# Performance work log

Measured on AMD Instinct MI355X. Metric: run time of the kernel, lower is better.

## Reference

```python
import jax, jax.numpy as jnp
import numpy as np

SR = 22050
HOP = 512
BINS_PER_OCTAVE = 24
N_OCTAVES = 7
N_BINS = BINS_PER_OCTAVE * N_OCTAVES  # 168
FMIN = 32.7  # center_bins with bins_per_semitone=1 leaves fmin unchanged


def _make_cqt_kernels():
    """Right-aligned (causal) complex CQT kernels, 24 bins/octave, 7 octaves.

    This is the explicit math the stateful SlidingCqt24 C++ routine computes
    incrementally: for each bin k with center freq f_k = fmin * 2^(k/24),
    a Hann-windowed complex exponential of length N_k = ceil(Q*sr/f_k),
    Q = 1/(2^(1/24)-1). Bins are ordered ascending in frequency, matching the
    per-octave np.flip layout of the original forward.
    """
    Q = 1.0 / (2.0 ** (1.0 / BINS_PER_OCTAVE) - 1.0)
    freqs = FMIN * 2.0 ** (np.arange(N_BINS) / BINS_PER_OCTAVE)
    lens = np.ceil(Q * SR / freqs).astype(np.int64)
    n_max = int(lens.max())  # 23014
    kr = np.zeros((N_BINS, n_max), dtype=np.float32)
    ki = np.zeros((N_BINS, n_max), dtype=np.float32)
    for k in range(N_BINS):  # small fixed loop over 168 bins (setup only)
        n = int(lens[k])
        t = np.arange(n)
        win = np.hanning(n)
        c = win * np.exp(2j * np.pi * freqs[k] * t / SR) / n
        kr[k, n_max - n:] = c.real.astype(np.float32)
        ki[k, n_max - n:] = c.imag.astype(np.float32)
    return kr, ki


def setup_inputs() -> dict:
    key = jax.random.key(0)
    audio = jax.random.normal(key, (4, 1, 352768), dtype=jnp.float32)
    kr, ki = _make_cqt_kernels()
    return {
        "audio_waveforms": audio,
        "kern_real": jnp.asarray(kr),
        "kern_imag": jnp.asarray(ki),
    }


def reference(audio_waveforms, kern_real, kern_imag):
    # audio: [B, C, S]; kernels: [K, Nmax]
    n_max = kern_real.shape[1]
    B, C, S = audio_waveforms.shape
    n_blocks = S // HOP  # 689
    # Causal sliding window: block i analyzes the n_max samples ending at
    # sample (i+1)*HOP (left zero-pad for early blocks), matching the
    # block-streaming behavior of the sliding CQT.
    pad = n_max - HOP
    x = jnp.pad(audio_waveforms, ((0, 0), (0, 0), (pad, 0)))
    # Strided frame gather: [n_blocks, Nmax] index table.
    idx = jnp.arange(n_blocks)[:, None] * HOP + jnp.arange(n_max)[None, :]
    frames = x[..., idx]  # [B, C, T, Nmax]
    re = jnp.einsum("bctn,kn->bctk", frames, kern_real)
    im = jnp.einsum("bctn,kn->bctk", frames, kern_imag)
    mag = jnp.sqrt(re * re + im * im)  # [B, C, n_blocks, n_bins]
    return mag
```

## Files before the change

### kernel.cpp

```cpp
#include <hip/hip_runtime.h>
#include <math.h>


namespace {
constexpr int kSR    = 22050;
constexpr int kHop   = 512;
constexpr int kBins  = 168;
constexpr int kT     = 689;
constexpr int kB     = 4;
constexpr int kS     = 352768;
constexpr float kKScale    = 4096.0f;
constexpr float kKScaleInv = 1.0f / 4096.0f;
constexpr int kG16 = 11;
constexpr int kAcc = kB * kT * kBins * 2;
constexpr int kTPadB   = 768;
constexpr int kBinPadB = 176;
constexpr int kAccB    = kB * kTPadB * kBinPadB * 2;
}

typedef _Float16 half8 __attribute__((ext_vector_type(8)));
typedef _Float16 half2v __attribute__((ext_vector_type(2)));
typedef float floatx4 __attribute__((ext_vector_type(4)));

struct Jobs {
  int k0[48];
  int lo[48];
  int hi[48];
  int n;
};

struct JobsC {
  int lo16[kG16];
  int cb16[kG16];
  int mlo[3];
  int sm[12];
  int slo[12];
  int shi[12];
  int ns;
  int totch;
};

__device__ inline void atomAddF(float* p, float v) {
  __hip_atomic_fetch_add(p, v, __ATOMIC_RELAXED, __HIP_MEMORY_SCOPE_AGENT);
}

typedef __attribute__((address_space(3))) unsigned int lds_uint;
typedef __attribute__((address_space(1))) const unsigned int glb_uint;
__device__ __forceinline__ void dma16(const void* g, void* l) {
  __builtin_amdgcn_global_load_lds((glb_uint*)g, (lds_uint*)l, 16, 0, 0);
}

__global__ __launch_bounds__(256) void prep_fused(
    const float* __restrict__ x, const float* __restrict__ kr,
    const float* __restrict__ ki, _Float16* __restrict__ xp,
    _Float16* __restrict__ bp, float* __restrict__ accb,
    const int pad, const int xps, const int nmax,
    const int nbx, const int nbp, const JobsC jt) {
  int bid = blockIdx.x;
  const int tid = threadIdx.x;

  if (bid < nbx) {
    const int halfx = xps >> 1;
    const int gid = bid * 256 + tid;
    if (gid >= kB * halfx) return;
    const int b = gid / halfx;
    const int i = (gid - b * halfx) * 2;
    float v0 = 0.f, v1 = 0.f;
    if (i     >= pad && i     < pad + kS) v0 = x[(size_t)b * kS + (i - pad)];
    if (i + 1 >= pad && i + 1 < pad + kS) v1 = x[(size_t)b * kS + (i + 1 - pad)];
    half2v h; h.x = (_Float16)v0; h.y = (_Float16)v1;
    *(half2v*)&xp[(size_t)b * xps + i] = h;
    return;
  }
  bid -= nbx;

  if (bid < nbp) {
    const int chunkid = bid * 4 + (tid >> 6);
    const int lane = tid & 63;
    if (chunkid >= jt.totch) return;
    int g = 0;
    #pragma unroll
    for (int j = 1; j < kG16; ++j)
      if (chunkid >= jt.cb16[j]) g = j;
    const int c = chunkid - jt.cb16[g];
    const int mm = lane & 15;
    const int q  = lane >> 4;
    const int bin  = g * 16 + mm;
    const int col0 = jt.lo16[g] + c * 32 + q * 8;
    const bool binok = (bin < kBins);
    const float* rowr = kr + (size_t)bin * nmax;
    const float* rowi = ki + (size_t)bin * nmax;
    half8 hre, him;
    #pragma unroll
    for (int j = 0; j < 8; ++j) {
      const int col = col0 + j;
      const bool ok = binok && (col < nmax);
      hre[j] = ok ? (_Float16)(rowr[col] * kKScale) : (_Float16)0.f;
      him[j] = ok ? (_Float16)(rowi[col] * kKScale) : (_Float16)0.f;
    }
    _Float16* dst = bp + (size_t)chunkid * 1024 + lane * 8;
    *(half8*)dst = hre;
    *(half8*)(dst + 512) = him;
    return;
  }
  bid -= nbp;

  const int idx = (bid * 256 + tid) * 4;
  if (idx < kAcc)
    *(floatx4*)&accb[idx] = (floatx4){0.f, 0.f, 0.f, 0.f};
}

__global__ __launch_bounds__(256) void cqt_mfma7(
    const _Float16* __restrict__ bp, const _Float16* __restrict__ xp,
    float* __restrict__ accb, const int xps, const JobsC jt) {
  __shared__ _Float16 lds[2][12288];

  const int sx = blockIdx.y;
  const int fb = blockIdx.x >> 2;
  const int b  = blockIdx.x & 3;
  const int tid  = threadIdx.x;
  const int wave = tid >> 6;
  const int lane = tid & 63;
  const int mm = lane & 15;
  const int q  = lane >> 4;
  const int mac = jt.sm[sx];
  const int g16 = mac * 4 + wave;
  const bool gvalid = (g16 < kG16);
  const int mlo = jt.mlo[mac];
  const int gs = gvalid ? ((jt.lo16[g16] - mlo) >> 5) : 0x7fffffff;
  const int slo = jt.slo[sx];
  const int shi = jt.shi[sx];
  const int fbase = fb * 64;

  const _Float16* xb = xp + (size_t)b * xps;
  const int i0 = wave * 2;
  int aoff[2];
  #pragma unroll
  for (int j = 0; j < 2; ++j) {
    const int idx = i0 + j;
    const int tl = idx & 3;
    int row = fbase + tl * 16 + mm;
    if (row > kT - 1) row = kT - 1;
    aoff[j] = row * kHop + q * 8 + ((idx >> 2) * 32);
  }
  const _Float16* bgrp =
      gvalid ? (bp + (size_t)(jt.cb16[g16] - gs) * 1024 + lane * 8) : bp;

  floatx4 accr[4], acci[4];
  #pragma unroll
  for (int tl = 0; tl < 4; ++tl) {
    accr[tl] = (floatx4){0.f, 0.f, 0.f, 0.f};
    acci[tl] = (floatx4){0.f, 0.f, 0.f, 0.f};
  }

  auto stageDMA = [&](int c, int buf) {
    _Float16* L = lds[buf];
    #pragma unroll
    for (int j = 0; j < 2; ++j)
      dma16(xb + mlo + c * 32 + aoff[j], L + (i0 + j) * 512);
    if (gvalid && c >= gs) {
      const _Float16* bs = bgrp + (size_t)c * 1024;
      #pragma unroll
      for (int cc = 0; cc < 2; ++cc)
        #pragma unroll
        for (int ri = 0; ri < 2; ++ri)
          dma16(bs + cc * 1024 + ri * 512,
                L + 4096 + (wave * 4 + cc * 2 + ri) * 512);
    }
  };

  auto compute = [&](int c, int buf) {
    if (!gvalid || c < gs) return;
    const _Float16* L = lds[buf];
    #pragma unroll
    for (int cc = 0; cc < 2; ++cc) {
      const half8 Bre = *(const half8*)(L + 4096 + (wave * 4 + cc * 2) * 512 + lane * 8);
      const half8 Bim = *(const half8*)(L + 4096 + (wave * 4 + cc * 2 + 1) * 512 + lane * 8);
      #pragma unroll
      for (int tl = 0; tl < 4; ++tl) {
        const half8 A = *(const half8*)(L + (cc * 4 + tl) * 512 + lane * 8);
        accr[tl] = __builtin_amdgcn_mfma_f32_16x16x32_f16(A, Bre, accr[tl], 0, 0, 0);
        acci[tl] = __builtin_amdgcn_mfma_f32_16x16x32_f16(A, Bim, acci[tl], 0, 0, 0);
      }
    }
  };

  stageDMA(slo, 0);
  int buf = 0;
  #pragma unroll 1
  for (int c = slo; c < shi; c += 2) {
    __syncthreads();
    if (c + 2 < shi) stageDMA(c + 2, buf ^ 1);
    compute(c, buf);
    buf ^= 1;
  }

  const int bin = g16 * 16 + mm;
  if (bin < kBins) {
    #pragma unroll
    for (int tl = 0; tl < 4; ++tl) {
      const int tb = fbase + tl * 16 + q * 4;
      #pragma unroll
      for (int r = 0; r < 4; ++r) {
        const int t = tb + r;
        if (t < kT) {
          const size_t o = (((size_t)b * kT + t) * kBins + bin) * 2;
          atomAddF(&accb[o],     accr[tl][r] * kKScaleInv);
          atomAddF(&accb[o + 1], acci[tl][r] * kKScaleInv);
        }
      }
    }
  }
}

__global__ __launch_bounds__(256) void cqt_mag_final(
    const float* __restrict__ accb, float* __restrict__ out,
    const int tp, const int kp) {
  int gid = blockIdx.x * 256 + threadIdx.x;
  if (gid >= kB * kT * kBins) return;
  const int k = gid % kBins;
  const int r = gid / kBins;
  const int t = r % kT;
  const int b = r / kT;
  const float2 v = ((const float2*)accb)[((size_t)b * tp + t) * kp + k];
  out[gid] = sqrtf(v.x * v.x + v.y * v.y);
}

__global__ __launch_bounds__(256) void prep_x_kernel(
    const float* __restrict__ x, _Float16* __restrict__ xp,
    const int pad, const int xps) {
  const int halfx = xps >> 1;
  int gid = blockIdx.x * 256 + threadIdx.x;
  if (gid >= kB * halfx) return;
  const int b = gid / halfx;
  const int i = (gid - b * halfx) * 2;
  float v0 = 0.f, v1 = 0.f;
  if (i     >= pad && i     < pad + kS) v0 = x[(size_t)b * kS + (i - pad)];
  if (i + 1 >= pad && i + 1 < pad + kS) v1 = x[(size_t)b * kS + (i + 1 - pad)];
  half2v h; h.x = (_Float16)v0; h.y = (_Float16)v1;
  *(half2v*)&xp[(size_t)b * xps + i] = h;
}

__global__ __launch_bounds__(256) void cqt_mfma_kernel(
    const float* __restrict__ kr, const float* __restrict__ ki,
    const _Float16* __restrict__ xp, float* __restrict__ accb,
    const int nmax, const int xps, const Jobs jt) {
  __shared__ _Float16 Bs[2][16][264];
  const int jb = blockIdx.x;
  const int k0   = jt.k0[jb];
  const int n_lo = jt.lo[jb];
  const int n_hi = jt.hi[jb];
  const int b  = blockIdx.z;
  const int fb = blockIdx.y;
  const int tid  = threadIdx.x;
  const int lane = tid & 63;
  const int wave = tid >> 6;
  const int m = lane & 15;
  const int q = lane >> 4;
  const int sbin = tid >> 4;
  const int scol = tid & 15;
  const int gbin = k0 + sbin;
  const bool binok = (gbin < kBins);
  const float* rowr = kr + (size_t)gbin * nmax;
  const float* rowi = ki + (size_t)gbin * nmax;
  const int fbase = fb * 256 + wave * 64;
  const _Float16* ax =
      xp + (size_t)b * xps + (size_t)(fbase + m) * kHop + q * 8;
  floatx4 accr[4], acci[4];
  #pragma unroll
  for (int tl = 0; tl < 4; ++tl) {
    accr[tl] = (floatx4){0.f, 0.f, 0.f, 0.f};
    acci[tl] = (floatx4){0.f, 0.f, 0.f, 0.f};
  }
  for (int n0r = n_lo; n0r < n_hi; n0r += 256) {
    __syncthreads();
    #pragma unroll
    for (int c = 0; c < 16; ++c) {
      const int col = n0r + scol + c * 16;
      const bool ok = binok && (col < nmax);
      const float vr = ok ? rowr[col] : 0.f;
      const float vi = ok ? rowi[col] : 0.f;
      Bs[0][sbin][scol + c * 16] = (_Float16)(vr * kKScale);
      Bs[1][sbin][scol + c * 16] = (_Float16)(vi * kKScale);
    }
    __syncthreads();
    const _Float16* axr = ax + n0r;
    #pragma unroll
    for (int c = 0; c < 8; ++c) {
      const int ko = c * 32 + q * 8;
      const half8 br = *(const half8*)&Bs[0][m][ko];
      const half8 bi = *(const half8*)&Bs[1][m][ko];
      #pragma unroll
      for (int tl = 0; tl < 4; ++tl) {
        const half8 a = *(const half8*)(axr + tl * 16 * kHop + c * 32);
        accr[tl] = __builtin_amdgcn_mfma_f32_16x16x32_f16(a, br, accr[tl], 0, 0, 0);
        acci[tl] = __builtin_amdgcn_mfma_f32_16x16x32_f16(a, bi, acci[tl], 0, 0, 0);
      }
    }
  }
  #pragma unroll
  for (int tl = 0; tl < 4; ++tl) {
    #pragma unroll
    for (int rr = 0; rr < 4; ++rr) {
      const int t = fbase + tl * 16 + q * 4 + rr;
      const size_t o = (((size_t)b * kTPadB + t) * kBinPadB + (k0 + m)) * 2;
      atomAddF(&accb[o],     accr[tl][rr] * kKScaleInv);
      atomAddF(&accb[o + 1], acci[tl][rr] * kKScaleInv);
    }
  }
}

namespace fb32 {
constexpr int TT = 8;
constexpr int KG = 4;
constexpr int kTTiles  = (kT + TT - 1) / TT;
constexpr int kKGroups = kBins / KG;
constexpr int kWaves   = kB * kTTiles * kKGroups;
}

__global__ __launch_bounds__(256) void cqt_mag_kernel(
    const float* __restrict__ x,
    const float* __restrict__ kr,
    const float* __restrict__ ki,
    float* __restrict__ out,
    const int nmax, const int pad) {
  using namespace fb32;
  const int wave = (blockIdx.x << 2) + (threadIdx.x >> 6);
  const int lane = threadIdx.x & 63;
  if (wave >= kWaves) return;
  const int kg    = wave / (kB * kTTiles);
  const int rem   = wave - kg * (kB * kTTiles);
  const int b     = rem / kTTiles;
  const int ttile = rem - b * kTTiles;
  const int k0 = kg * KG;
  const int t0 = ttile * TT;
  const double Q  = 1.0 / (exp2(1.0 / 24.0) - 1.0);
  const double f0 = 32.7 * exp2((double)k0 / 24.0);
  int N = (int)ceil(Q * (double)kSR / f0) + 8;
  int full_start = nmax - N;
  if (full_start < 0) full_start = 0;
  int tbase[TT], lo[TT], t_last;
  { int t = t0 + TT - 1; if (t > kT - 1) t = kT - 1; t_last = t; }
  #pragma unroll
  for (int tt = 0; tt < TT; ++tt) {
    int t = t0 + tt; if (t > kT - 1) t = kT - 1;
    tbase[tt] = b * kS + t * kHop - pad;
    lo[tt]    = pad - t * kHop;
  }
  int head_start = pad - t_last * kHop;
  if (head_start < full_start) head_start = full_start;
  int safe = pad - t0 * kHop;
  if (safe < head_start) safe = head_start;
  int body_start = nmax - ((nmax - safe) & ~63);
  float accr[TT][KG], acci[TT][KG];
  #pragma unroll
  for (int tt = 0; tt < TT; ++tt)
    #pragma unroll
    for (int kk = 0; kk < KG; ++kk) { accr[tt][kk] = 0.f; acci[tt][kk] = 0.f; }
  for (int n = body_start - 64; n > head_start - 64; n -= 64) {
    const int nn = n + lane;
    const bool kok = (nn >= 0);
    float krv[KG], kiv[KG];
    #pragma unroll
    for (int kk = 0; kk < KG; ++kk) {
      krv[kk] = kok ? kr[(k0 + kk) * nmax + nn] : 0.f;
      kiv[kk] = kok ? ki[(k0 + kk) * nmax + nn] : 0.f;
    }
    float a[TT];
    #pragma unroll
    for (int tt = 0; tt < TT; ++tt)
      a[tt] = (nn >= lo[tt]) ? x[tbase[tt] + nn] : 0.f;
    #pragma unroll
    for (int tt = 0; tt < TT; ++tt)
      #pragma unroll
      for (int kk = 0; kk < KG; ++kk) {
        accr[tt][kk] = fmaf(a[tt], krv[kk], accr[tt][kk]);
        acci[tt][kk] = fmaf(a[tt], kiv[kk], acci[tt][kk]);
      }
  }
  for (int n = body_start; n < nmax; n += 64) {
    const int nn = n + lane;
    float krv[KG], kiv[KG];
    #pragma unroll
    for (int kk = 0; kk < KG; ++kk) {
      krv[kk] = kr[(k0 + kk) * nmax + nn];
      kiv[kk] = ki[(k0 + kk) * nmax + nn];
    }
    float a[TT];
    #pragma unroll
    for (int tt = 0; tt < TT; ++tt)
      a[tt] = x[tbase[tt] + nn];
    #pragma unroll
    for (int tt = 0; tt < TT; ++tt)
      #pragma unroll
      for (int kk = 0; kk < KG; ++kk) {
        accr[tt][kk] = fmaf(a[tt], krv[kk], accr[tt][kk]);
        acci[tt][kk] = fmaf(a[tt], kiv[kk], acci[tt][kk]);
      }
  }
  #pragma unroll
  for (int tt = 0; tt < TT; ++tt) {
    #pragma unroll
    for (int kk = 0; kk < KG; ++kk) {
      float r = accr[tt][kk];
      float i = acci[tt][kk];
      #pragma unroll
      for (int s = 32; s > 0; s >>= 1) {
        r += __shfl_xor(r, s, 64);
        i += __shfl_xor(i, s, 64);
      }
      if (lane == 0) {
        const int t = t0 + tt;
        if (t < kT)
          out[(b * kT + t) * kBins + (k0 + kk)] = sqrtf(r * r + i * i);
      }
    }
  }
}

extern "C" void kernel_launch(void* const* d_in, const int* in_sizes, int n_in,
                              void* d_out, int out_size, void* d_ws, size_t ws_size,
                              hipStream_t stream) {
  const float* x  = (const float*)d_in[0];
  const float* kr = (const float*)d_in[1];
  const float* ki = (const float*)d_in[2];
  float* out = (float*)d_out;

  const int nmax = in_sizes[1] / kBins;
  const int pad  = nmax - kHop;

  const int kcap = ((nmax + 255) / 256) * 256;
  const double Q = 1.0 / (exp2(1.0 / 24.0) - 1.0);

  JobsC jc;
  int tot = 0;
  for (int g = 0; g < kG16; ++g) {
    const double f0 = 32.7 * exp2((double)(16 * g) / 24.0);
    const int N = (int)ceil(Q * (double)kSR / f0) + 8;
    int lo = nmax - N;
    if (lo < 0) lo = 0;
    lo &= ~255;
    jc.lo16[g] = lo;
    jc.cb16[g] = tot;
    tot += (kcap - lo) / 32;
  }
  jc.totch = tot;
  int ns = 0;
  for (int m = 0; m < 3; ++m) {
    jc.mlo[m] = jc.lo16[4 * m];
    const int C = (kcap - jc.mlo[m]) / 32;
    const int nsl = (C + 95) / 96;
    const int len = ((C + nsl - 1) / nsl + 1) & ~1;
    for (int s = 0; s < nsl && ns < 12; ++s) {
      const int lo = s * len;
      if (lo >= C) break;
      int hi = lo + len;
      if (hi > C) hi = C;
      jc.sm[ns] = m; jc.slo[ns] = lo; jc.shi[ns] = hi;
      ++ns;
    }
  }
  jc.ns = ns;

  const int xpsA = (kT - 1) * kHop + kcap + 256;
  const size_t xpA_bytes = (size_t)kB * xpsA * sizeof(_Float16);
  const size_t accA_off  = (xpA_bytes + 511) & ~(size_t)511;
  const size_t accA_bytes = (size_t)kAcc * sizeof(float);
  const size_t bpA_off   = (accA_off + accA_bytes + 511) & ~(size_t)511;
  const size_t bpA_bytes = (size_t)tot * 2048;
  const size_t ws_A = bpA_off + bpA_bytes;

  const int xpsB = (kTPadB - 1) * kHop + kcap + 256;
  const size_t xpB_bytes = (size_t)kB * xpsB * sizeof(_Float16);
  const size_t accB_off  = (xpB_bytes + 511) & ~(size_t)511;
  const size_t accB_bytes = (size_t)kAccB * sizeof(float);
  const size_t ws_B = accB_off + accB_bytes;

  if (ws_size >= ws_A) {
    _Float16* xp = (_Float16*)d_ws;
    float* accb  = (float*)((char*)d_ws + accA_off);
    _Float16* bp = (_Float16*)((char*)d_ws + bpA_off);

    const int nbx = (kB * (xpsA / 2) + 255) / 256;
    const int nbp = (tot + 3) / 4;
    const int nba = (kAcc / 4 + 255) / 256;
    prep_fused<<<nbx + nbp + nba, 256, 0, stream>>>(
        x, kr, ki, xp, bp, accb, pad, xpsA, nmax, nbx, nbp, jc);

    {
      dim3 grid(44, ns);
      cqt_mfma7<<<grid, 256, 0, stream>>>(bp, xp, accb, xpsA, jc);
    }
    {
      const int total = kB * kT * kBins;
      cqt_mag_final<<<(total + 255) / 256, 256, 0, stream>>>(
          accb, out, kT, kBins);
    }
    return;
  }

  if (ws_size >= ws_B) {
    _Float16* xp = (_Float16*)d_ws;
    float* accb  = (float*)((char*)d_ws + accB_off);
    Jobs jt;
    int nj = 0;
    for (int g = 0; g < 11; ++g) {
      const int gk0 = 16 * g;
      const double f0 = 32.7 * exp2((double)gk0 / 24.0);
      const int N = (int)ceil(Q * (double)kSR / f0) + 8;
      int lo = nmax - N;
      if (lo < 0) lo = 0;
      lo = (lo / 2048) * 2048;
      for (int s = lo; s < kcap && nj < 48; s += 2048) {
        jt.k0[nj] = gk0;
        jt.lo[nj] = s;
        jt.hi[nj] = (s + 2048 < kcap) ? s + 2048 : kcap;
        ++nj;
      }
    }
    jt.n = nj;
    hipMemsetAsync(accb, 0, accB_bytes, stream);
    {
      const int total = kB * (xpsB / 2);
      prep_x_kernel<<<(total + 255) / 256, 256, 0, stream>>>(x, xp, pad, xpsB);
    }
    {
      dim3 grid(nj, kTPadB / 256, kB);
      cqt_mfma_kernel<<<grid, 256, 0, stream>>>(kr, ki, xp, accb, nmax, xpsB, jt);
    }
    {
      const int total = kB * kT * kBins;
      cqt_mag_final<<<(total + 255) / 256, 256, 0, stream>>>(
          accb, out, kTPadB, kBinPadB);
    }
    return;
  }

  {
    const int blocks = fb32::kWaves / 4;
    cqt_mag_kernel<<<blocks, 256, 0, stream>>>(x, kr, ki, out, nmax, pad);
  }
}
```

Measured before the change: 129.2 us.

## Fuse magnitude epilogue into MFMA kernel via last-block counter and rebalance slices

Removes the separate magnitude kernel launch: each column of blocks increments a per-column counter after its atomic accumulations, and the last block to finish computes sqrt(re^2+im^2) for that 64-frame tile and writes the output. The counter array is zeroed alongside the accumulator in the prep kernel. The K-dimension slicing per macro group is also changed to fixed counts (15, 3, 1), raising the number of y-slices to about 19 so the grid has more blocks and the per-group work is more even. This costs a threadfence plus counter atomic per block and more atomic contention on the accumulator.

```diff
diff --git a/kernel.cpp b/kernel.cpp
--- a/kernel.cpp
+++ b/kernel.cpp
@@ -13,6 +13,7 @@
 constexpr float kKScaleInv = 1.0f / 4096.0f;
 constexpr int kG16 = 11;
 constexpr int kAcc = kB * kT * kBins * 2;
+constexpr int kCnt = 64;
 constexpr int kTPadB   = 768;
 constexpr int kBinPadB = 176;
 constexpr int kAccB    = kB * kTPadB * kBinPadB * 2;
@@ -33,9 +34,9 @@
   int lo16[kG16];
   int cb16[kG16];
   int mlo[3];
-  int sm[12];
-  int slo[12];
-  int shi[12];
+  int sm[24];
+  int slo[24];
+  int shi[24];
   int ns;
   int totch;
 };
@@ -106,14 +107,16 @@
   bid -= nbp;
 
   const int idx = (bid * 256 + tid) * 4;
-  if (idx < kAcc)
+  if (idx < kAcc + kCnt)
     *(floatx4*)&accb[idx] = (floatx4){0.f, 0.f, 0.f, 0.f};
 }
 
-__global__ __launch_bounds__(256) void cqt_mfma7(
+__global__ __launch_bounds__(256) void cqt_mfma8(
     const _Float16* __restrict__ bp, const _Float16* __restrict__ xp,
-    float* __restrict__ accb, const int xps, const JobsC jt) {
+    float* __restrict__ accb, int* __restrict__ cnt,
+    float* __restrict__ out, const int xps, const JobsC jt) {
   __shared__ _Float16 lds[2][12288];
+  __shared__ int lastFlag;
 
   const int sx = blockIdx.y;
   const int fb = blockIdx.x >> 2;
@@ -208,6 +211,32 @@
           atomAddF(&accb[o],     accr[tl][r] * kKScaleInv);
           atomAddF(&accb[o + 1], acci[tl][r] * kKScaleInv);
         }
+      }
+    }
+  }
+
+  __threadfence();
+  __syncthreads();
+  if (tid == 0) {
+    const int old = __hip_atomic_fetch_add(&cnt[blockIdx.x], 1,
+                                           __ATOMIC_ACQ_REL,
+                                           __HIP_MEMORY_SCOPE_AGENT);
+    lastFlag = (old == (int)gridDim.y - 1);
+  }
+  __syncthreads();
+  if (lastFlag) {
+    __threadfence();
+    #pragma unroll 1
+    for (int i = tid; i < 64 * kBins; i += 256) {
+      const int t = fbase + i / kBins;
+      const int k = i - (i / kBins) * kBins;
+      if (t < kT) {
+        const size_t o = (((size_t)b * kT + t) * kBins + k) * 2;
+        const float re = __hip_atomic_load(&accb[o], __ATOMIC_RELAXED,
+                                           __HIP_MEMORY_SCOPE_AGENT);
+        const float im = __hip_atomic_load(&accb[o + 1], __ATOMIC_RELAXED,
+                                           __HIP_MEMORY_SCOPE_AGENT);
+        out[o >> 1] = sqrtf(re * re + im * im);
       }
     }
   }
@@ -445,13 +474,14 @@
     tot += (kcap - lo) / 32;
   }
   jc.totch = tot;
+  const int nsl_m[3] = {15, 3, 1};
   int ns = 0;
   for (int m = 0; m < 3; ++m) {
     jc.mlo[m] = jc.lo16[4 * m];
     const int C = (kcap - jc.mlo[m]) / 32;
-    const int nsl = (C + 95) / 96;
+    const int nsl = nsl_m[m];
     const int len = ((C + nsl - 1) / nsl + 1) & ~1;
-    for (int s = 0; s < nsl && ns < 12; ++s) {
+    for (int s = 0; s < nsl && ns < 24; ++s) {
       const int lo = s * len;
       if (lo >= C) break;
       int hi = lo + len;
@@ -465,7 +495,7 @@
   const int xpsA = (kT - 1) * kHop + kcap + 256;
   const size_t xpA_bytes = (size_t)kB * xpsA * sizeof(_Float16);
   const size_t accA_off  = (xpA_bytes + 511) & ~(size_t)511;
-  const size_t accA_bytes = (size_t)kAcc * sizeof(float);
+  const size_t accA_bytes = (size_t)(kAcc + kCnt) * sizeof(float);
   const size_t bpA_off   = (accA_off + accA_bytes + 511) & ~(size_t)511;
   const size_t bpA_bytes = (size_t)tot * 2048;
   const size_t ws_A = bpA_off + bpA_bytes;
@@ -479,22 +509,18 @@
   if (ws_size >= ws_A) {
     _Float16* xp = (_Float16*)d_ws;
     float* accb  = (float*)((char*)d_ws + accA_off);
+    int* cnt     = (int*)(accb + kAcc);
     _Float16* bp = (_Float16*)((char*)d_ws + bpA_off);
 
     const int nbx = (kB * (xpsA / 2) + 255) / 256;
     const int nbp = (tot + 3) / 4;
-    const int nba = (kAcc / 4 + 255) / 256;
+    const int nba = ((kAcc + kCnt) / 4 + 255) / 256;
     prep_fused<<<nbx + nbp + nba, 256, 0, stream>>>(
         x, kr, ki, xp, bp, accb, pad, xpsA, nmax, nbx, nbp, jc);
 
     {
       dim3 grid(44, ns);
-      cqt_mfma7<<<grid, 256, 0, stream>>>(bp, xp, accb, xpsA, jc);
-    }
-    {
-      const int total = kB * kT * kBins;
-      cqt_mag_final<<<(total + 255) / 256, 256, 0, stream>>>(
-          accb, out, kT, kBins);
+      cqt_mfma8<<<grid, 256, 0, stream>>>(bp, xp, accb, cnt, out, xpsA, jc);
     }
     return;
   }
```

After: 213.0 us. +64.9%, slower.
